# Performance work log

Measured on AMD Instinct MI355X. Metric: run time of the kernel, lower is better.

## Reference

```python
import jax, jax.numpy as jnp
import numpy as np
from jax import lax

DN = ('NCHW', 'OIHW', 'NCHW')


def conv2d(x, w, b, stride, pad):
    y = lax.conv_general_dilated(x, w, (stride, stride), [(pad, pad), (pad, pad)],
                                 dimension_numbers=DN)
    return y + b[None, :, None, None]


def conv2d_transpose(x, w, b):
    # k=4, s=2, p=1 transposed conv: lhs_dilation=2, padding k-1-p=2.
    # w is stored directly as OIHW for this dilated conv (reference params).
    y = lax.conv_general_dilated(x, w, (1, 1), [(2, 2), (2, 2)],
                                 lhs_dilation=(2, 2), dimension_numbers=DN)
    return y + b[None, :, None, None]


def setup_inputs() -> dict:
    key = jax.random.key(0)
    ks = jax.random.split(key, 16)
    D, K = 64, 512  # embedding_dim, num_embeddings
    C1, C2 = 128, 256

    def w(k, shape, fan_in):
        return (jax.random.normal(k, shape, jnp.float32) / np.sqrt(fan_in)).astype(jnp.float32)

    inp = {
        'x':   jax.random.normal(ks[0], (8, 3, 256, 256), jnp.float32),
        # encoder: two stride-2 conv stages (k=4,s=2,p=1) + ReLU
        'ew1': w(ks[1], (C1, 3, 4, 4), 3 * 16),   'eb1': jnp.zeros((C1,), jnp.float32),
        'ew2': w(ks[2], (C2, C1, 4, 4), C1 * 16), 'eb2': jnp.zeros((C2,), jnp.float32),
        # pre_vq 1x1 conv: C2 -> D
        'pvw': w(ks[3], (D, C2, 1, 1), C2),       'pvb': jnp.zeros((D,), jnp.float32),
        # codebook, uniform(-1/K, 1/K) as in the torch init
        'emb': jax.random.uniform(ks[4], (K, D), jnp.float32, -1.0 / K, 1.0 / K),
        # post_vq 3x3 conv: D -> C2
        'qvw': w(ks[5], (C2, D, 3, 3), D * 9),    'qvb': jnp.zeros((C2,), jnp.float32),
        # decoder: two stride-2 transposed conv stages
        'dw1': w(ks[6], (C1, C2, 4, 4), C2 * 16), 'db1': jnp.zeros((C1,), jnp.float32),
        'dw2': w(ks[7], (3, C1, 4, 4), C1 * 16),  'db2': jnp.zeros((3,), jnp.float32),
    }
    return inp


def vector_quantize(z_e, emb, commitment_cost):
    # z_e: [B, D, H, W] -> [B, H, W, D]
    inputs = jnp.transpose(z_e, (0, 2, 3, 1))
    B, H, W, D = inputs.shape
    K = emb.shape[0]
    flat = inputs.reshape(-1, D)                                   # [N, D]
    dist = (jnp.sum(flat * flat, axis=1, keepdims=True)
            + jnp.sum(emb * emb, axis=1)
            - 2.0 * jnp.matmul(flat, emb.T))                        # [N, K]
    idx = jnp.argmin(dist, axis=1)                                  # [N]
    encodings = jax.nn.one_hot(idx, K, dtype=flat.dtype)            # [N, K]
    quantized = emb[idx].reshape(B, H, W, D)                        # gather == encodings @ emb

    e_latent_loss = jnp.mean((lax.stop_gradient(quantized) - inputs) ** 2)
    q_latent_loss = jnp.mean((quantized - lax.stop_gradient(inputs)) ** 2)
    loss = q_latent_loss + commitment_cost * e_latent_loss

    quantized_st = inputs + lax.stop_gradient(quantized - inputs)   # straight-through
    avg_probs = jnp.mean(encodings, axis=0)
    perplexity = jnp.exp(-jnp.sum(avg_probs * jnp.log(avg_probs + 1e-10)))
    return loss, jnp.transpose(quantized_st, (0, 3, 1, 2)), perplexity, encodings


def reference(x, ew1, eb1, ew2, eb2, pvw, pvb, emb, qvw, qvb, dw1, db1, dw2, db2):
    commitment_cost = 0.25
    # encode
    h = jax.nn.relu(conv2d(x, ew1, eb1, 2, 1))    # [8,128,128,128]
    h = jax.nn.relu(conv2d(h, ew2, eb2, 2, 1))    # [8,256,64,64]
    z_e = conv2d(h, pvw, pvb, 1, 0)               # [8,64,64,64]
    # vector quantize
    loss, quantized, perplexity, _ = vector_quantize(z_e, emb, commitment_cost)
    # decode
    g = conv2d(quantized, qvw, qvb, 1, 1)         # [8,256,64,64]
    g = jax.nn.relu(conv2d_transpose(g, dw1, db1))  # [8,128,128,128]
    x_recon = conv2d_transpose(g, dw2, db2)       # [8,3,256,256]
    return (loss, x_recon, perplexity)
```

## Files before the change

### kernel.cpp

```cpp
#include <hip/hip_runtime.h>
#include <math.h>

typedef unsigned short u16;
typedef unsigned int uint;
typedef __attribute__((ext_vector_type(8))) short bh8;
typedef __attribute__((ext_vector_type(4))) float f32x4;

#define DEV __device__ __forceinline__

DEV u16 f2bf(float x) {
  uint u = __builtin_bit_cast(uint, x);
  return (u16)((u + 0x7FFFu + ((u >> 16) & 1u)) >> 16);
}
DEV float bf2f(u16 h) { return __builtin_bit_cast(float, (uint)h << 16); }

DEV int xcd_swz(int bid, int nb) {
  int c = nb >> 3;
  return (bid & 7) * c + (bid >> 3);
}

__global__ __launch_bounds__(256, 4) void conv1_f32(const float* __restrict__ src,
                                                    const float* __restrict__ Bt,
                                                    const float* __restrict__ bias,
                                                    uint* __restrict__ outu) {
  __shared__ __align__(16) float As[16*64];
  __shared__ __align__(16) float Bs[16*64];

  const int t = threadIdx.x;
  const int bid = (int)blockIdx.x;
  const int nt = bid & 1, m = bid >> 1;
  const int pl = t & 63, kb = t >> 6;
  const int p = m*64 + pl;
  const int n = p >> 14, h = (p >> 7) & 127, w = p & 127;
  const int ti = t & 15, tj = t >> 4;

  float acc[4][4];
  #pragma unroll
  for (int i = 0; i < 4; ++i)
    #pragma unroll
    for (int j = 0; j < 4; ++j) acc[i][j] = 0.f;

  for (int k0 = 0; k0 < 48; k0 += 16) {
    #pragma unroll
    for (int jj = 0; jj < 4; ++jj) {
      int kr = jj*4 + kb, k = k0 + kr;
      int ic = k >> 4, r = k & 15;
      int ih = 2*h - 1 + (r >> 2), iw = 2*w - 1 + (r & 3);
      As[kr*64 + pl] = ((unsigned)ih < 256u && (unsigned)iw < 256u)
        ? src[((n*3 + ic) << 16) + (ih << 8) + iw] : 0.f;
    }
    {
      int kr = t >> 4, c4 = t & 15;
      ((float4*)Bs)[kr*16 + c4] =
          *((const float4*)(Bt + (size_t)(k0 + kr)*128 + nt*64) + c4);
    }
    __syncthreads();
    #pragma unroll
    for (int kk = 0; kk < 16; ++kk) {
      float a[4], b[4];
      *(float4*)&a[0] = *(const float4*)&As[kk*64 + ti*4];
      *(float4*)&b[0] = *(const float4*)&Bs[kk*64 + tj*4];
      #pragma unroll
      for (int i = 0; i < 4; ++i)
        #pragma unroll
        for (int j = 0; j < 4; ++j)
          acc[i][j] += a[i]*b[j];
    }
    __syncthreads();
  }

  const int nn = m >> 8, hh = (m >> 1) & 127;
  const int woff2 = (m & 1) * 32;
  #pragma unroll
  for (int j = 0; j < 4; ++j) {
    const int oc = nt*64 + tj*4 + j;
    uint pk[4];
    #pragma unroll
    for (int q = 0; q < 4; ++q) {
      float v = fmaxf(acc[q][j] + bias[oc], 0.f);
      u16 hi = f2bf(v);
      u16 lo = f2bf(v - bf2f(hi));
      pk[q] = (uint)hi | ((uint)lo << 16);
    }
    uint* bp = outu + (size_t)(nn*128 + oc)*16384 + hh*128;
    *(uint2*)(bp + woff2 + ti*2)      = make_uint2(pk[0], pk[2]);
    *(uint2*)(bp + 64 + woff2 + ti*2) = make_uint2(pk[1], pk[3]);
  }
}

__global__ __launch_bounds__(256, 2) void conv2_mfma3(const uint* __restrict__ h1u,
                                                      const u16* __restrict__ Bh,
                                                      const u16* __restrict__ Bl,
                                                      const float* __restrict__ bias,
                                                      float* __restrict__ out) {
  __shared__ __align__(16) u16 Ah[128*72 + 32];
  __shared__ __align__(16) u16 Al[128*72 + 32];
  __shared__ __align__(16) u16 Bhs[128*72 + 32];
  __shared__ __align__(16) u16 Bls[128*72 + 32];

  const int t = threadIdx.x;
  const int bid = xcd_swz((int)blockIdx.x, (int)gridDim.x);
  const int nt = bid & 1, mt = bid >> 1;
  const int pl = t & 127, kb = t >> 7;
  const int p = mt*128 + pl;
  const int n = p >> 12, h = (p >> 6) & 63, w = p & 63;
  const int lane = t & 63, wv = t >> 6;
  const int lr = lane & 15, lg = lane >> 4;
  const int wm = wv & 1, wn = wv >> 1;

  int off[4]; uint mskd[4];
  off[0] = 64 + w - 1; mskd[0] = (w >= 1)  ? ~0u : 0u;
  off[1] = w;          mskd[1] = ~0u;
  off[2] = 64 + w;     mskd[2] = ~0u;
  off[3] = w + 1;      mskd[3] = (w <= 62) ? ~0u : 0u;

  f32x4 acc[4][4];
  #pragma unroll
  for (int fm = 0; fm < 4; ++fm)
    #pragma unroll
    for (int fn = 0; fn < 4; ++fn)
      #pragma unroll
      for (int q = 0; q < 4; ++q) acc[fm][fn][q] = 0.f;

  const int aw = pl*72 + kb*32;

  for (int k0 = 0; k0 < 2048; k0 += 64) {
    const int dy = k0 >> 9, icb = (k0 >> 2) & 127;
    const int ih = 2*h - 1 + dy;
    const uint mih = ((unsigned)ih < 128u) ? ~0u : 0u;
    const uint* pb = h1u + (size_t)(n*128 + icb + kb*8)*16384
                        + (((unsigned)ih < 128u) ? ih : 0)*128;
    uint m2[4];
    #pragma unroll
    for (int dx = 0; dx < 4; ++dx) m2[dx] = mskd[dx] & mih;

    uint raw[32];
    #pragma unroll
    for (int c = 0; c < 8; ++c)
      #pragma unroll
      for (int dx = 0; dx < 4; ++dx)
        raw[c*4 + dx] = pb[c*16384 + off[dx]] & m2[dx];

    uint hi16[16], lo16[16];
    #pragma unroll
    for (int q = 0; q < 16; ++q) {
      uint a = raw[2*q], b = raw[2*q+1];
      hi16[q] = (a & 0xffffu) | (b << 16);
      lo16[q] = (a >> 16) | (b & 0xffff0000u);
    }
    __syncthreads();
    #pragma unroll
    for (int i = 0; i < 4; ++i) {
      *(uint4*)&Ah[aw + i*8] = *(uint4*)&hi16[4*i];
      *(uint4*)&Al[aw + i*8] = *(uint4*)&lo16[4*i];
    }
    #pragma unroll
    for (int i = 0; i < 4; ++i) {
      int id = i*256 + t, oc = id >> 3, ch = id & 7;
      size_t bo = (size_t)(nt*128 + oc)*2048 + k0 + ch*8;
      *(uint4*)&Bhs[oc*72 + ch*8] = *(const uint4*)(Bh + bo);
      *(uint4*)&Bls[oc*72 + ch*8] = *(const uint4*)(Bl + bo);
    }
    __syncthreads();

    #pragma unroll
    for (int ks = 0; ks < 2; ++ks) {
      bh8 afh[4], afl[4];
      #pragma unroll
      for (int fm = 0; fm < 4; ++fm) {
        const int r = (wm*64 + fm*16 + lr)*72 + ks*32 + lg*8;
        afh[fm] = *(const bh8*)&Ah[r];
        afl[fm] = *(const bh8*)&Al[r];
      }
      #pragma unroll
      for (int fn = 0; fn < 4; ++fn) {
        const int r = (wn*64 + fn*16 + lr)*72 + ks*32 + lg*8;
        bh8 bfh = *(const bh8*)&Bhs[r];
        bh8 bfl = *(const bh8*)&Bls[r];
        #pragma unroll
        for (int fm = 0; fm < 4; ++fm) {
          acc[fm][fn] = __builtin_amdgcn_mfma_f32_16x16x32_bf16(afh[fm], bfh, acc[fm][fn], 0,0,0);
          acc[fm][fn] = __builtin_amdgcn_mfma_f32_16x16x32_bf16(afl[fm], bfh, acc[fm][fn], 0,0,0);
          acc[fm][fn] = __builtin_amdgcn_mfma_f32_16x16x32_bf16(afh[fm], bfl, acc[fm][fn], 0,0,0);
        }
      }
    }
  }

  #pragma unroll
  for (int fm = 0; fm < 4; ++fm) {
    const int pq = mt*128 + wm*64 + fm*16 + lg*4;
    const int nn = pq >> 12, hwq = pq & 4095;
    #pragma unroll
    for (int fn = 0; fn < 4; ++fn) {
      const int oc = nt*128 + wn*64 + fn*16 + lr;
      const float bv = bias[oc];
      float v0 = fmaxf(acc[fm][fn][0] + bv, 0.f);
      float v1 = fmaxf(acc[fm][fn][1] + bv, 0.f);
      float v2 = fmaxf(acc[fm][fn][2] + bv, 0.f);
      float v3 = fmaxf(acc[fm][fn][3] + bv, 0.f);
      *(float4*)(out + (((size_t)(nn*256 + oc)) << 12) + hwq) = make_float4(v0,v1,v2,v3);
    }
  }
}

__global__ __launch_bounds__(256, 3) void prevq_vq(const float* __restrict__ h2,
                                                   const float* __restrict__ btp,
                                                   const float* __restrict__ pvb,
                                                   const float* __restrict__ emb,
                                                   const float* __restrict__ Et,
                                                   const float* __restrict__ enrm,
                                                   uint* __restrict__ qz32,
                                                   int* __restrict__ hist,
                                                   float* __restrict__ loss_sum) {
  __shared__ __align__(16) float SM[10944 + 16];
  float* Zs   = SM;
  float* As   = SM + 4352;
  float* Bs   = SM + 4352 + 1024;
  float* Es   = SM + 4352;
  float* nrmS = SM + 4352 + 4224;
  float* redv = SM + 4352 + 4224 + 128;
  int*   redi = (int*)(redv + 1088);
  int*   sIdx = (int*)(redv + 2176);

  const int t = threadIdx.x;
  const int base = (int)blockIdx.x * 64;
  const int n = base >> 12, hwb = base & 4095;
  const int ti = t & 15, tj = t >> 4;

  {
    const int pl = t & 63, kb = t >> 6;
    const int hw = hwb + pl;
    float acc[4][4];
    #pragma unroll
    for (int i = 0; i < 4; ++i)
      #pragma unroll
      for (int j = 0; j < 4; ++j) acc[i][j] = 0.f;

    for (int k0 = 0; k0 < 256; k0 += 16) {
      #pragma unroll
      for (int jj = 0; jj < 4; ++jj) {
        int kr = jj*4 + kb;
        As[kr*64 + pl] = h2[((size_t)(n*256 + k0 + kr) << 12) + hw];
      }
      {
        int kr = t >> 4, c4 = t & 15;
        ((float4*)Bs)[kr*16 + c4] = *((const float4*)(btp + (size_t)(k0 + kr)*64) + c4);
      }
      __syncthreads();
      #pragma unroll
      for (int kk = 0; kk < 16; ++kk) {
        float a[4], b[4];
        *(float4*)&a[0] = *(const float4*)&As[kk*64 + ti*4];
        *(float4*)&b[0] = *(const float4*)&Bs[kk*64 + tj*4];
        #pragma unroll
        for (int i = 0; i < 4; ++i)
          #pragma unroll
          for (int j = 0; j < 4; ++j)
            acc[i][j] += a[i]*b[j];
      }
      __syncthreads();
    }
    #pragma unroll
    for (int j = 0; j < 4; ++j) {
      float bv = pvb[tj*4 + j];
      #pragma unroll
      for (int i = 0; i < 4; ++i)
        Zs[(tj*4 + j)*68 + ti*4 + i] = acc[i][j] + bv;
    }
  }

  float bv[4]; int bi[4];
  #pragma unroll
  for (int i = 0; i < 4; ++i) { bv[i] = 3.402823466e38f; bi[i] = 0; }

  for (int c = 0; c < 4; ++c) {
    float acc[4][8];
    #pragma unroll
    for (int i = 0; i < 4; ++i)
      #pragma unroll
      for (int j = 0; j < 8; ++j) acc[i][j] = 0.f;

    for (int hh = 0; hh < 2; ++hh) {
      __syncthreads();
      #pragma unroll
      for (int i = 0; i < 4; ++i) {
        int fid = i*256 + t, row = fid >> 5, c4 = fid & 31;
        *(float4*)&Es[row*132 + c4*4] =
            *(const float4*)(Et + (size_t)(hh*32 + row)*512 + c*128 + c4*4);
      }
      if (hh == 0 && t < 128) nrmS[t] = enrm[c*128 + t];
      __syncthreads();
      #pragma unroll 4
      for (int kk = 0; kk < 32; ++kk) {
        float4 a0 = *(const float4*)&Zs[(hh*32 + kk)*68 + ti*4];
        float4 b0 = *(const float4*)&Es[kk*132 + tj*8];
        float4 b1 = *(const float4*)&Es[kk*132 + tj*8 + 4];
        float a[4] = {a0.x, a0.y, a0.z, a0.w};
        float b[8] = {b0.x,b0.y,b0.z,b0.w, b1.x,b1.y,b1.z,b1.w};
        #pragma unroll
        for (int i = 0; i < 4; ++i)
          #pragma unroll
          for (int j = 0; j < 8; ++j)
            acc[i][j] += a[i]*b[j];
      }
    }
    #pragma unroll
    for (int j = 0; j < 8; ++j) {
      int code = c*128 + tj*8 + j;
      float nv = nrmS[tj*8 + j];
      #pragma unroll
      for (int i = 0; i < 4; ++i) {
        float d = nv - 2.f*acc[i][j];
        if (d < bv[i]) { bv[i] = d; bi[i] = code; }
      }
    }
  }

  __syncthreads();
  #pragma unroll
  for (int i = 0; i < 4; ++i) {
    redv[(ti*4 + i)*17 + tj] = bv[i];
    redi[(ti*4 + i)*17 + tj] = bi[i];
  }
  __syncthreads();
  if (t < 64) {
    float best = 3.402823466e38f; int bid = 0x7fffffff;
    #pragma unroll
    for (int j = 0; j < 16; ++j) {
      float v = redv[t*17 + j]; int ix = redi[t*17 + j];
      if (v < best || (v == best && ix < bid)) { best = v; bid = ix; }
    }
    sIdx[t] = bid;
  }
  __syncthreads();

  const int px = t & 63, grp = t >> 6;
  const int ix = sIdx[px];
  const float* er = emb + (size_t)ix * 64 + grp*16;
  uint* qb = qz32 + ((size_t)(n*32 + grp*8))*4096 + hwb + px;
  float ls = 0.f;
  #pragma unroll
  for (int dp = 0; dp < 8; ++dp) {
    float e0 = er[2*dp], e1 = er[2*dp + 1];
    float z0 = Zs[(grp*16 + 2*dp)*68 + px];
    float z1 = Zs[(grp*16 + 2*dp + 1)*68 + px];
    float d0 = e0 - z0, d1 = e1 - z1;
    ls += d0*d0 + d1*d1;
    qb[(size_t)dp * 4096] = (uint)f2bf(e0) | ((uint)f2bf(e1) << 16);
  }
  if (t < 64) atomicAdd(&hist[ix], 1);
  #pragma unroll
  for (int o = 32; o; o >>= 1) ls += __shfl_down(ls, o, 64);
  if ((t & 63) == 0) atomicAdd(loss_sum, ls);
}

__global__ void finalize_kernel(const int* __restrict__ hist,
                                const float* __restrict__ loss_sum,
                                float* __restrict__ out_loss,
                                float* __restrict__ out_perp) {
  __shared__ float red[512];
  int t = threadIdx.x;
  float pr = (float)hist[t] * (1.f/32768.f);
  red[t] = pr * logf(pr + 1e-10f);
  __syncthreads();
  for (int s = 256; s; s >>= 1) {
    if (t < s) red[t] += red[t + s];
    __syncthreads();
  }
  if (t == 0) {
    out_loss[0] = 1.25f * loss_sum[0] * (1.f/2097152.f);
    out_perp[0] = expf(-red[0]);
  }
}

enum { M_POSTVQ, M_DECONV1, M_DECONV2 };

template<int MODE>
__global__ __launch_bounds__(256, 4) void dec_mfma128(const uint* __restrict__ srcu,
                                                      const u16* __restrict__ Bt,
                                                      const float* __restrict__ bias,
                                                      uint* __restrict__ out32) {
  constexpr int K = (MODE == M_POSTVQ) ? 576 : 1024;
  __shared__ __align__(16) u16 As[128*72 + 32];
  __shared__ __align__(16) u16 Bs[128*72 + 32];

  const int t = threadIdx.x;
  int bid = xcd_swz((int)blockIdx.x, (int)gridDim.x);
  int par = 0, nt = 0, mt;
  if constexpr (MODE == M_DECONV1) { par = bid & 3; mt = bid >> 2; }
  else                             { nt = bid & 1;  mt = bid >> 1; }
  const u16* Brow = Bt + (size_t)((MODE == M_DECONV1) ? par*128 : nt*128) * K;

  const int pl = t & 127, kb = t >> 7;
  const int p = mt*128 + pl;
  const int n = p >> 12, h = (p >> 6) & 63, w = p & 63;
  const int lane = t & 63, wv = t >> 6;
  const int lr = lane & 15, lg = lane >> 4;
  const int wm = wv & 1, wn = wv >> 1;

  f32x4 acc[4][4];
  #pragma unroll
  for (int fm = 0; fm < 4; ++fm)
    #pragma unroll
    for (int fn = 0; fn < 4; ++fn)
      #pragma unroll
      for (int q = 0; q < 4; ++q) acc[fm][fn][q] = 0.f;

  const int aw = pl*72 + kb*32;

  for (int k0 = 0; k0 < K; k0 += 64) {
    const uint* up; bool ok;
    if constexpr (MODE == M_POSTVQ) {
      int r = k0 >> 6, kh = r / 3, kw = r - 3*kh;
      int ih = h - 1 + kh, iw = w - 1 + kw;
      ok = ((unsigned)ih < 64u) && ((unsigned)iw < 64u);
      up = srcu + ((size_t)(n*32 + kb*16)) * 4096
                + (ok ? ((ih << 6) + iw) : 0);
    } else {
      int j = k0 >> 8, icb = k0 & 255;
      int j1 = j >> 1, j0 = j & 1;
      int py = par >> 1, px = par & 1;
      int ih = h + py - 1 + j1, iw = w + px - 1 + j0;
      ok = ((unsigned)ih < 64u) && ((unsigned)iw < 64u);
      up = srcu + ((size_t)(n*128 + (icb >> 1) + kb*16)) * 4096
                + (ok ? ((ih << 6) + iw) : 0);
    }
    uint raw[16];
    #pragma unroll
    for (int i = 0; i < 16; ++i)
      raw[i] = ok ? up[(size_t)i * 4096] : 0u;

    __syncthreads();
    #pragma unroll
    for (int i = 0; i < 4; ++i)
      *(uint4*)&As[aw + i*8] =
          make_uint4(raw[4*i], raw[4*i+1], raw[4*i+2], raw[4*i+3]);

    #pragma unroll
    for (int i = 0; i < 4; ++i) {
      int id = i*256 + t, oc = id >> 3, ch = id & 7;
      *(uint4*)&Bs[oc*72 + ch*8] = *(const uint4*)(Brow + (size_t)oc*K + k0 + ch*8);
    }
    __syncthreads();

    #pragma unroll
    for (int ks = 0; ks < 2; ++ks) {
      bh8 af[4];
      #pragma unroll
      for (int fm = 0; fm < 4; ++fm)
        af[fm] = *(const bh8*)&As[(wm*64 + fm*16 + lr)*72 + ks*32 + lg*8];
      #pragma unroll
      for (int fn = 0; fn < 4; ++fn) {
        bh8 bf = *(const bh8*)&Bs[(wn*64 + fn*16 + lr)*72 + ks*32 + lg*8];
        #pragma unroll
        for (int fm = 0; fm < 4; ++fm)
          acc[fm][fn] = __builtin_amdgcn_mfma_f32_16x16x32_bf16(af[fm], bf, acc[fm][fn], 0, 0, 0);
      }
    }
  }

  const bool evn = !(lr & 1);
  #pragma unroll
  for (int fm = 0; fm < 4; ++fm) {
    const int pq = mt*128 + wm*64 + fm*16 + lg*4;
    const int nn = pq >> 12, hwq = pq & 4095;
    #pragma unroll
    for (int fn = 0; fn < 4; ++fn) {
      const int oc = nt*128 + wn*64 + fn*16 + lr;
      const float bvv = bias[oc];
      float v[4];
      #pragma unroll
      for (int q = 0; q < 4; ++q) {
        v[q] = acc[fm][fn][q] + bvv;
        if constexpr (MODE == M_DECONV1) v[q] = fmaxf(v[q], 0.f);
      }
      float pv[4];
      #pragma unroll
      for (int q = 0; q < 4; ++q) pv[q] = __shfl_xor(v[q], 1, 64);
      uint pk[4];
      #pragma unroll
      for (int q = 0; q < 4; ++q) {
        u16 a = f2bf(evn ? v[q] : pv[q]);
        u16 b = f2bf(evn ? pv[q] : v[q]);
        pk[q] = (uint)a | ((uint)b << 16);
      }
      size_t pbase;
      if constexpr (MODE == M_POSTVQ)
        pbase = ((size_t)(nn*128 + (oc >> 1))) * 4096 + hwq;
      else
        pbase = ((size_t)((nn*4 + par)*64 + (oc >> 1))) * 4096 + hwq;
      if (evn) *(uint2*)(out32 + pbase)     = make_uint2(pk[0], pk[1]);
      else     *(uint2*)(out32 + pbase + 2) = make_uint2(pk[2], pk[3]);
    }
  }
}

__global__ __launch_bounds__(256, 4) void deconv2_mfma(const uint* __restrict__ srcu,
                                                       const u16* __restrict__ Bt,
                                                       const float* __restrict__ bias,
                                                       float* __restrict__ outf) {
  constexpr int K = 512, BN = 16;
  __shared__ __align__(16) u16 As[128 * 72];
  __shared__ __align__(16) u16 Bs[BN * 72];

  const int t = threadIdx.x;
  int bid = xcd_swz((int)blockIdx.x, (int)gridDim.x);
  int par = bid & 3; bid >>= 2;
  const int mt = bid;
  const u16* Brow = Bt + (size_t)par * BN * K;

  const int pl = t & 127, kb = t >> 7;
  const int p = mt * 128 + pl;
  const int n = p >> 14, h = (p >> 7) & 127, w = p & 127;

  const int lane = t & 63, wv = t >> 6;
  const int lr = lane & 15, lg = lane >> 4;

  f32x4 acc[2];
  #pragma unroll
  for (int fm = 0; fm < 2; ++fm)
    #pragma unroll
    for (int q = 0; q < 4; ++q) acc[fm][q] = 0.f;

  for (int k0 = 0; k0 < K; k0 += 64) {
    int tap = k0 >> 7, icb = k0 & 127;
    int j1 = tap >> 1, j0 = tap & 1;
    int qy = par >> 1, qx = par & 1;
    int ih = h - 1 + qy + j1, iw = w - 1 + qx + j0;
    bool ok = ((unsigned)ih < 128u) && ((unsigned)iw < 128u);
    int ipar = ((ih & 1) << 1) | (iw & 1);
    const uint* up = srcu + ((size_t)((n*4 + ipar)*64 + (icb >> 1) + kb*16)) * 4096
                          + (ok ? (((ih >> 1) << 6) + (iw >> 1)) : 0);
    uint raw[16];
    #pragma unroll
    for (int i = 0; i < 16; ++i)
      raw[i] = ok ? up[(size_t)i * 4096] : 0u;

    __syncthreads();
    #pragma unroll
    for (int i = 0; i < 4; ++i)
      *(uint4*)&As[pl*72 + kb*32 + i*8] =
          make_uint4(raw[4*i], raw[4*i+1], raw[4*i+2], raw[4*i+3]);
    {
      int id = t;
      if (id < BN*8) {
        int oc = id >> 3, ch = id & 7;
        *(uint4*)&Bs[oc*72 + ch*8] = *(const uint4*)(Brow + (size_t)oc*K + k0 + ch*8);
      }
    }
    __syncthreads();

    #pragma unroll
    for (int ks = 0; ks < 2; ++ks) {
      bh8 af[2];
      #pragma unroll
      for (int fm = 0; fm < 2; ++fm)
        af[fm] = *(const bh8*)&As[(wv*32 + fm*16 + lr)*72 + ks*32 + lg*8];
      bh8 bf = *(const bh8*)&Bs[lr*72 + ks*32 + lg*8];
      #pragma unroll
      for (int fm = 0; fm < 2; ++fm)
        acc[fm] = __builtin_amdgcn_mfma_f32_16x16x32_bf16(af[fm], bf, acc[fm], 0, 0, 0);
    }
  }

  #pragma unroll
  for (int fm = 0; fm < 2; ++fm) {
    const int pq = mt*128 + wv*32 + fm*16 + lg*4;
    const int oc = lr;
    if (oc < 3) {
      const float bvv = bias[oc];
      const int nn = pq >> 14;
      const int hq = (pq >> 7) & 127, wq = pq & 127;
      const int qy = par >> 1, qx = par & 1;
      const int oh = 2*hq + qy;
      float* ob = outf + (((size_t)(nn*3 + oc)) << 16) + (oh << 8) + qx;
      ob[2*wq]     = acc[fm][0] + bvv;
      ob[2*wq + 2] = acc[fm][1] + bvv;
      ob[2*wq + 4] = acc[fm][2] + bvv;
      ob[2*wq + 6] = acc[fm][3] + bvv;
    }
  }
}

__global__ void prep_enc(const float* __restrict__ ew1, const float* __restrict__ ew2,
                         const float* __restrict__ pvw, const float* __restrict__ emb,
                         float* bt1, u16* bt2h, u16* bt2l, float* btp,
                         float* Et, float* enrm) {
  int i = blockIdx.x * 256 + threadIdx.x;
  if (i < 6144) {
    int k = i >> 7, oc = i & 127;
    bt1[i] = ew1[oc*48 + k];
  } else if ((i -= 6144) < 524288) {
    int oc = i >> 11, k = i & 2047;
    int dy = k >> 9, ic = (k >> 2) & 127, dx = k & 3;
    float v = ew2[oc*2048 + ic*16 + dy*4 + dx];
    u16 hi = f2bf(v);
    bt2h[i] = hi;
    bt2l[i] = f2bf(v - bf2f(hi));
  } else if ((i -= 524288) < 16384) {
    int k = i >> 6, oc = i & 63;
    btp[i] = pvw[oc*256 + k];
  } else if ((i -= 16384) < 32768) {
    int d = i >> 9, code = i & 511;
    Et[i] = emb[code*64 + d];
  } else if ((i -= 32768) < 512) {
    float s = 0.f;
    const float* er = emb + (size_t)i * 64;
    #pragma unroll
    for (int d = 0; d < 64; ++d) s += er[d]*er[d];
    enrm[i] = s;
  }
}

__global__ void prep_dec(const float* __restrict__ qvw, const float* __restrict__ dw1,
                         const float* __restrict__ dw2,
                         u16* btq, u16* btd, u16* btd2) {
  int i = blockIdx.x * 256 + threadIdx.x;
  if (i < 147456) {
    int oc = i / 576, rem = i - oc*576, r = rem >> 6, ic = rem & 63;
    btq[i] = f2bf(qvw[oc*576 + ic*9 + r]);
  } else if ((i -= 147456) < 524288) {
    int pr = i >> 17, oc = (i >> 10) & 127, j = (i >> 8) & 3, ic = i & 255;
    int py = pr >> 1, px = pr & 1, j1 = j >> 1, j0 = j & 1;
    btd[i] = f2bf(dw1[oc*4096 + ic*16 + (py + 2*j1)*4 + (px + 2*j0)]);
  } else if ((i -= 524288) < 32768) {
    int q = i >> 13, oc = (i >> 9) & 15, tap = (i >> 7) & 3, ic = i & 127;
    int qy = q >> 1, qx = q & 1, j1 = tap >> 1, j0 = tap & 1;
    btd2[i] = (oc < 3) ? f2bf(dw2[oc*2048 + ic*16 + (qy + 2*j1)*4 + (qx + 2*j0)]) : (u16)0;
  }
}

extern "C" void kernel_launch(void* const* d_in, const int* in_sizes, int n_in,
                              void* d_out, int out_size, void* d_ws, size_t ws_size,
                              hipStream_t stream) {
  (void)in_sizes; (void)n_in; (void)ws_size;
  const float* x   = (const float*)d_in[0];
  const float* ew1 = (const float*)d_in[1];
  const float* eb1 = (const float*)d_in[2];
  const float* ew2 = (const float*)d_in[3];
  const float* eb2 = (const float*)d_in[4];
  const float* pvw = (const float*)d_in[5];
  const float* pvb = (const float*)d_in[6];
  const float* emb = (const float*)d_in[7];
  const float* qvw = (const float*)d_in[8];
  const float* qvb = (const float*)d_in[9];
  const float* dw1 = (const float*)d_in[10];
  const float* db1 = (const float*)d_in[11];
  const float* dw2 = (const float*)d_in[12];
  const float* db2 = (const float*)d_in[13];
  float* out = (float*)d_out;

  char* ws = (char*)d_ws;
  uint*  h1u  = (uint*) (ws);
  float* h2   = (float*)(ws + 67108864);
  uint*  qz32 = (uint*) (ws + 109051904);
  int*   hist = (int*)  (ws + 113246208);
  float* lsum = (float*)(ws + 113248256);
  float* bt1  = (float*)(ws + 113248320);
  float* btp  = (float*)(ws + 113272896);
  u16*   bt2h = (u16*)  (ws + 113338432);
  u16*   bt2l = (u16*)  (ws + 114387008);
  u16*   btq  = (u16*)  (ws + 115435584);
  u16*   btd  = (u16*)  (ws + 115730496);
  u16*   btd2 = (u16*)  (ws + 116779072);
  float* Et   = (float*)(ws + 116844608);
  float* enrm = (float*)(ws + 116975680);
  uint* g32  = (uint*)(ws + 67108864);
  uint* g232 = (uint*)ws;

  hipMemsetAsync(hist, 0, 2048 + 64, stream);
  prep_enc<<<2266, 256, 0, stream>>>(ew1, ew2, pvw, emb, bt1, bt2h, bt2l, btp, Et, enrm);
  prep_dec<<<2752, 256, 0, stream>>>(qvw, dw1, dw2, btq, btd, btd2);

  conv1_f32<<<4096, 256, 0, stream>>>(x, bt1, eb1, h1u);
  conv2_mfma3<<<512, 256, 0, stream>>>(h1u, bt2h, bt2l, eb2, h2);

  prevq_vq<<<512, 256, 0, stream>>>(h2, btp, pvb, emb, Et, enrm, qz32, hist, lsum);
  finalize_kernel<<<1, 512, 0, stream>>>(hist, lsum, out, out + (out_size - 1));

  dec_mfma128<M_POSTVQ> <<<512,  256, 0, stream>>>(qz32, btq, qvb, g32);
  dec_mfma128<M_DECONV1><<<1024, 256, 0, stream>>>(g32, btd, db1, g232);
  deconv2_mfma<<<4096, 256, 0, stream>>>(g232, btd2, db2, out + 1);
}
```

Before: 399.5 us.

## Compute VQ codebook distances with split-bf16 MFMA instead of scalar FP32 FMAs

The VQ nearest-code search in prevq_vq now splits z and the codebook into bf16 hi/lo pairs and runs three bf16 MFMAs per tile (hi*hi, lo*hi, hi*lo) in place of the scalar fp32 outer-product loop. Codebook prep now writes row-major bf16 hi/lo arrays instead of a transposed fp32 array. The argmin reduction uses wavefront shuffles followed by a small cross-wave reduction. Shared memory grows to about 74KB and launch bounds drop to 2 blocks per SM. The split-bf16 approximation can change which code wins when two distances are nearly tied.

```diff
diff --git a/kernel.cpp b/kernel.cpp
--- a/kernel.cpp
+++ b/kernel.cpp
@@ -204,24 +204,28 @@
   }
 }
 
-__global__ __launch_bounds__(256, 3) void prevq_vq(const float* __restrict__ h2,
+__global__ __launch_bounds__(256, 2) void prevq_vq(const float* __restrict__ h2,
                                                    const float* __restrict__ btp,
                                                    const float* __restrict__ pvb,
                                                    const float* __restrict__ emb,
-                                                   const float* __restrict__ Et,
+                                                   const u16* __restrict__ Ebh,
+                                                   const u16* __restrict__ Ebl,
                                                    const float* __restrict__ enrm,
                                                    uint* __restrict__ qz32,
                                                    int* __restrict__ hist,
                                                    float* __restrict__ loss_sum) {
-  __shared__ __align__(16) float SM[10944 + 16];
-  float* Zs   = SM;
-  float* As   = SM + 4352;
-  float* Bs   = SM + 4352 + 1024;
-  float* Es   = SM + 4352;
-  float* nrmS = SM + 4352 + 4224;
-  float* redv = SM + 4352 + 4224 + 128;
-  int*   redi = (int*)(redv + 1088);
-  int*   sIdx = (int*)(redv + 2176);
+  __shared__ __align__(16) char SMEM[75776];
+  float* Zs    = (float*)SMEM;
+  u16*   Zh    = (u16*)(SMEM + 17408);
+  u16*   Zl    = (u16*)(SMEM + 26624);
+  u16*   Eh    = (u16*)(SMEM + 35840);
+  u16*   El    = (u16*)(SMEM + 54272);
+  float* nrmS  = (float*)(SMEM + 72704);
+  float* wredv = (float*)(SMEM + 73216);
+  int*   wredi = (int*)(SMEM + 74240);
+  int*   sIdx  = (int*)(SMEM + 75264);
+  float* As    = (float*)(SMEM + 35840);
+  float* Bs    = (float*)(SMEM + 35840 + 4096);
 
   const int t = threadIdx.x;
   const int base = (int)blockIdx.x * 64;
@@ -263,72 +267,107 @@
     }
     #pragma unroll
     for (int j = 0; j < 4; ++j) {
-      float bv = pvb[tj*4 + j];
-      #pragma unroll
-      for (int i = 0; i < 4; ++i)
-        Zs[(tj*4 + j)*68 + ti*4 + i] = acc[i][j] + bv;
-    }
-  }
-
-  float bv[4]; int bi[4];
-  #pragma unroll
-  for (int i = 0; i < 4; ++i) { bv[i] = 3.402823466e38f; bi[i] = 0; }
+      const int d = tj*4 + j;
+      const float bvv = pvb[d];
+      #pragma unroll
+      for (int i = 0; i < 4; ++i) {
+        const int px = ti*4 + i;
+        float z = acc[i][j] + bvv;
+        Zs[d*68 + px] = z;
+        u16 h = f2bf(z);
+        Zh[px*72 + d] = h;
+        Zl[px*72 + d] = f2bf(z - bf2f(h));
+      }
+    }
+  }
+
+  const int lane = t & 63, wv = t >> 6;
+  const int lr = lane & 15, lg = lane >> 4;
+
+  float bv2[4][4]; int bi2[4][4];
+  #pragma unroll
+  for (int fm = 0; fm < 4; ++fm)
+    #pragma unroll
+    for (int q = 0; q < 4; ++q) { bv2[fm][q] = 3.402823466e38f; bi2[fm][q] = 0; }
 
   for (int c = 0; c < 4; ++c) {
-    float acc[4][8];
-    #pragma unroll
-    for (int i = 0; i < 4; ++i)
-      #pragma unroll
-      for (int j = 0; j < 8; ++j) acc[i][j] = 0.f;
-
-    for (int hh = 0; hh < 2; ++hh) {
-      __syncthreads();
-      #pragma unroll
-      for (int i = 0; i < 4; ++i) {
-        int fid = i*256 + t, row = fid >> 5, c4 = fid & 31;
-        *(float4*)&Es[row*132 + c4*4] =
-            *(const float4*)(Et + (size_t)(hh*32 + row)*512 + c*128 + c4*4);
-      }
-      if (hh == 0 && t < 128) nrmS[t] = enrm[c*128 + t];
-      __syncthreads();
-      #pragma unroll 4
-      for (int kk = 0; kk < 32; ++kk) {
-        float4 a0 = *(const float4*)&Zs[(hh*32 + kk)*68 + ti*4];
-        float4 b0 = *(const float4*)&Es[kk*132 + tj*8];
-        float4 b1 = *(const float4*)&Es[kk*132 + tj*8 + 4];
-        float a[4] = {a0.x, a0.y, a0.z, a0.w};
-        float b[8] = {b0.x,b0.y,b0.z,b0.w, b1.x,b1.y,b1.z,b1.w};
+    __syncthreads();
+    #pragma unroll
+    for (int i = 0; i < 4; ++i) {
+      int id = i*256 + t, row = id >> 3, ch = id & 7;
+      *(uint4*)&Eh[row*72 + ch*8] = *(const uint4*)(Ebh + (size_t)(c*128 + row)*64 + ch*8);
+      *(uint4*)&El[row*72 + ch*8] = *(const uint4*)(Ebl + (size_t)(c*128 + row)*64 + ch*8);
+    }
+    if (t < 128) nrmS[t] = enrm[c*128 + t];
+    __syncthreads();
+
+    f32x4 acc2[4][2];
+    #pragma unroll
+    for (int fm = 0; fm < 4; ++fm)
+      #pragma unroll
+      for (int fn = 0; fn < 2; ++fn)
         #pragma unroll
-        for (int i = 0; i < 4; ++i)
-          #pragma unroll
-          for (int j = 0; j < 8; ++j)
-            acc[i][j] += a[i]*b[j];
-      }
-    }
-    #pragma unroll
-    for (int j = 0; j < 8; ++j) {
-      int code = c*128 + tj*8 + j;
-      float nv = nrmS[tj*8 + j];
-      #pragma unroll
-      for (int i = 0; i < 4; ++i) {
-        float d = nv - 2.f*acc[i][j];
-        if (d < bv[i]) { bv[i] = d; bi[i] = code; }
-      }
-    }
-  }
-
-  __syncthreads();
-  #pragma unroll
-  for (int i = 0; i < 4; ++i) {
-    redv[(ti*4 + i)*17 + tj] = bv[i];
-    redi[(ti*4 + i)*17 + tj] = bi[i];
-  }
+        for (int q = 0; q < 4; ++q) acc2[fm][fn][q] = 0.f;
+
+    #pragma unroll
+    for (int ks = 0; ks < 2; ++ks) {
+      bh8 ah[4], al[4];
+      #pragma unroll
+      for (int fm = 0; fm < 4; ++fm) {
+        const int r = (fm*16 + lr)*72 + ks*32 + lg*8;
+        ah[fm] = *(const bh8*)&Zh[r];
+        al[fm] = *(const bh8*)&Zl[r];
+      }
+      #pragma unroll
+      for (int fn = 0; fn < 2; ++fn) {
+        const int r = (wv*32 + fn*16 + lr)*72 + ks*32 + lg*8;
+        bh8 bh_ = *(const bh8*)&Eh[r];
+        bh8 bl_ = *(const bh8*)&El[r];
+        #pragma unroll
+        for (int fm = 0; fm < 4; ++fm) {
+          acc2[fm][fn] = __builtin_amdgcn_mfma_f32_16x16x32_bf16(ah[fm], bh_, acc2[fm][fn], 0,0,0);
+          acc2[fm][fn] = __builtin_amdgcn_mfma_f32_16x16x32_bf16(al[fm], bh_, acc2[fm][fn], 0,0,0);
+          acc2[fm][fn] = __builtin_amdgcn_mfma_f32_16x16x32_bf16(ah[fm], bl_, acc2[fm][fn], 0,0,0);
+        }
+      }
+    }
+    #pragma unroll
+    for (int fn = 0; fn < 2; ++fn) {
+      const int code = c*128 + wv*32 + fn*16 + lr;
+      const float nv = nrmS[wv*32 + fn*16 + lr];
+      #pragma unroll
+      for (int fm = 0; fm < 4; ++fm)
+        #pragma unroll
+        for (int q = 0; q < 4; ++q) {
+          float d = nv - 2.f*acc2[fm][fn][q];
+          if (d < bv2[fm][q]) { bv2[fm][q] = d; bi2[fm][q] = code; }
+        }
+    }
+  }
+
+  #pragma unroll
+  for (int fm = 0; fm < 4; ++fm)
+    #pragma unroll
+    for (int q = 0; q < 4; ++q) {
+      float v = bv2[fm][q]; int ix = bi2[fm][q];
+      #pragma unroll
+      for (int m = 1; m < 16; m <<= 1) {
+        float ov = __shfl_xor(v, m, 64);
+        int   oi = __shfl_xor(ix, m, 64);
+        if (ov < v || (ov == v && oi < ix)) { v = ov; ix = oi; }
+      }
+      if (lr == 0) {
+        const int px = fm*16 + lg*4 + q;
+        wredv[wv*64 + px] = v;
+        wredi[wv*64 + px] = ix;
+      }
+    }
   __syncthreads();
   if (t < 64) {
     float best = 3.402823466e38f; int bid = 0x7fffffff;
     #pragma unroll
-    for (int j = 0; j < 16; ++j) {
-      float v = redv[t*17 + j]; int ix = redi[t*17 + j];
+    for (int w2 = 0; w2 < 4; ++w2) {
+      float v = wredv[w2*64 + t]; int ix = wredi[w2*64 + t];
       if (v < best || (v == best && ix < bid)) { best = v; bid = ix; }
     }
     sIdx[t] = bid;
@@ -586,7 +625,7 @@
 __global__ void prep_enc(const float* __restrict__ ew1, const float* __restrict__ ew2,
                          const float* __restrict__ pvw, const float* __restrict__ emb,
                          float* bt1, u16* bt2h, u16* bt2l, float* btp,
-                         float* Et, float* enrm) {
+                         u16* Ebh, u16* Ebl, float* enrm) {
   int i = blockIdx.x * 256 + threadIdx.x;
   if (i < 6144) {
     int k = i >> 7, oc = i & 127;
@@ -602,8 +641,10 @@
     int k = i >> 6, oc = i & 63;
     btp[i] = pvw[oc*256 + k];
   } else if ((i -= 16384) < 32768) {
-    int d = i >> 9, code = i & 511;
-    Et[i] = emb[code*64 + d];
+    float v = emb[i];
+    u16 hi = f2bf(v);
+    Ebh[i] = hi;
+    Ebl[i] = f2bf(v - bf2f(hi));
   } else if ((i -= 32768) < 512) {
     float s = 0.f;
     const float* er = emb + (size_t)i * 64;
@@ -664,19 +705,20 @@
   u16*   btq  = (u16*)  (ws + 115435584);
   u16*   btd  = (u16*)  (ws + 115730496);
   u16*   btd2 = (u16*)  (ws + 116779072);
-  float* Et   = (float*)(ws + 116844608);
+  u16*   Ebh  = (u16*)  (ws + 116844608);
+  u16*   Ebl  = (u16*)  (ws + 116910144);
   float* enrm = (float*)(ws + 116975680);
   uint* g32  = (uint*)(ws + 67108864);
   uint* g232 = (uint*)ws;
 
   hipMemsetAsync(hist, 0, 2048 + 64, stream);
-  prep_enc<<<2266, 256, 0, stream>>>(ew1, ew2, pvw, emb, bt1, bt2h, bt2l, btp, Et, enrm);
+  prep_enc<<<2266, 256, 0, stream>>>(ew1, ew2, pvw, emb, bt1, bt2h, bt2l, btp, Ebh, Ebl, enrm);
   prep_dec<<<2752, 256, 0, stream>>>(qvw, dw1, dw2, btq, btd, btd2);
 
   conv1_f32<<<4096, 256, 0, stream>>>(x, bt1, eb1, h1u);
   conv2_mfma3<<<512, 256, 0, stream>>>(h1u, bt2h, bt2l, eb2, h2);
 
-  prevq_vq<<<512, 256, 0, stream>>>(h2, btp, pvb, emb, Et, enrm, qz32, hist, lsum);
+  prevq_vq<<<512, 256, 0, stream>>>(h2, btp, pvb, emb, Ebh, Ebl, enrm, qz32, hist, lsum);
   finalize_kernel<<<1, 512, 0, stream>>>(hist, lsum, out, out + (out_size - 1));
 
   dec_mfma128<M_POSTVQ> <<<512,  256, 0, stream>>>(qz32, btq, qvb, g32);
```

Result: faster. 390.1 us (-2.4%).
